# Kernel optimization log

Measured on AMD Instinct MI355X. Metric: run time of the kernel, lower is better.

## Reference

```python
import jax, jax.numpy as jnp
import numpy as np

H = 4          # attention heads
K = 16         # knn neighbors
EPS = 1e-5     # BatchNorm eps


def setup_inputs() -> dict:
    key = jax.random.key(0)
    ks = jax.random.split(key, 10)
    B, C, T, N = 2, 128, 32, 512
    OUT = 128
    HID = 2 * C + 2 * OUT  # ff hidden = in*2 + out*2
    s = 0.02
    return {
        "x_all": jax.random.normal(ks[0], (B, C, T, N), jnp.float32),
        "Wq": jax.random.normal(ks[1], (C, C), jnp.float32) * s,
        "Wk": jax.random.normal(ks[2], (C, C), jnp.float32) * s,
        "Wv": jax.random.normal(ks[3], (C, C), jnp.float32) * s,
        "W1": jax.random.normal(ks[4], (HID, C), jnp.float32) * s,
        "W2": jax.random.normal(ks[5], (OUT, HID), jnp.float32) * s,
        "bn_gamma": 1.0 + 0.1 * jax.random.normal(ks[6], (OUT,), jnp.float32),
        "bn_beta": 0.1 * jax.random.normal(ks[7], (OUT,), jnp.float32),
        "bn_mean": 0.1 * jax.random.normal(ks[8], (OUT,), jnp.float32),
        "bn_var": jax.random.uniform(ks[9], (OUT,), jnp.float32, 0.5, 1.5),
    }


def reference(x_all, Wq, Wk, Wv, W1, W2, bn_gamma, bn_beta, bn_mean, bn_var):
    B, C, T, N = x_all.shape
    D = C // H
    # --- st_group_points: candidate pool = 3 consecutive frames (replicate temporal pad), frame-major ---
    xp = jnp.concatenate([x_all[:, :, :1], x_all, x_all[:, :, -1:]], axis=2)   # (B,C,T+2,N)
    pool = jnp.stack([xp[:, :, :-2], xp[:, :, 1:-1], xp[:, :, 2:]], axis=3)    # (B,C,T,3,N)
    pool = pool.reshape(B, C, T, 3 * N)                                        # (B,C,T,3N)
    # KNN on xyz (channels 0:3); sqrt is monotone so topk on squared dists gives same indices
    a = x_all[:, :3]                                                           # (B,3,T,N)
    b = pool[:, :3]                                                            # (B,3,T,3N)
    d2 = jnp.sum((a[..., :, None] - b[..., None, :]) ** 2, axis=1)             # (B,T,N,3N)
    _, idx = jax.lax.top_k(-d2, K)                                             # (B,T,N,K) smallest-dist
    nb = jnp.take_along_axis(pool[:, :, :, None, :], idx[:, None], axis=-1)    # (B,C,T,N,K)
    rel = x_all[..., None] - nb                                                # diff grouping (B,C,T,N,K)
    # --- per-point local attention over K neighbors (1x1 convs == channel matmuls), all t at once ---
    q = jnp.einsum('oc,bctn->botn', Wq, x_all).reshape(B, H, D, T, N)
    k = jnp.einsum('oc,bctnk->botnk', Wk, rel).reshape(B, H, D, T, N, K)
    v = jnp.einsum('oc,bctnk->botnk', Wv, rel).reshape(B, H, D, T, N, K)
    energy = jnp.einsum('bhdtn,bhdtnk->bhtnk', q, k) / jnp.sqrt(jnp.float32(D))
    attn = jax.nn.softmax(energy, axis=-1)                                     # (B,H,T,N,K)
    agg = jnp.einsum('bhtnk,bhdtnk->bhdtn', attn, v).reshape(B, C, T, N)
    # --- residual + BatchNorm1d (eval mode, running stats) + conv feed-forward ---
    h = x_all + agg
    scale = (bn_gamma / jnp.sqrt(bn_var + EPS))[None, :, None, None]
    h = (h - bn_mean[None, :, None, None]) * scale + bn_beta[None, :, None, None]
    h = jax.nn.leaky_relu(jnp.einsum('oc,bctn->botn', W1, h), 0.2)
    y = jnp.einsum('oc,bctn->botn', W2, h)                                     # (B,OUT,T,N)
    return jnp.concatenate([x_all[:, :4], y], axis=1)                          # (B,4+OUT,T,N)
```

## Files before the change

kernel.cpp:

```cpp
#include <hip/hip_runtime.h>
#include <hip/hip_bf16.h>

typedef __hip_bfloat16 bf16;
typedef unsigned long long u64;
typedef __attribute__((ext_vector_type(8))) short short8;
typedef __attribute__((ext_vector_type(4))) float f32x4;

#define B_   2
#define C_   128
#define T_   32
#define N_   512
#define K_   16
#define HID_ 512
#define TN   (T_*N_)
#define PTS  (B_*T_*N_)

#define MFMA_BF16(a,b,c) __builtin_amdgcn_mfma_f32_16x16x32_bf16((a),(b),(c),0,0,0)

__device__ __forceinline__ float b2f(bf16 v){ return __bfloat162float(v); }
__device__ __forceinline__ bf16  f2b(float v){ return __float2bfloat16(v); }
__device__ __forceinline__ float bqf(short v){
  return __uint_as_float(((unsigned)(unsigned short)v) << 16);
}

__device__ __forceinline__ float ldc(const void* p, int i, bool f32) {
  return f32 ? ((const float*)p)[i] : b2f(((const bf16*)p)[i]);
}

__global__ __launch_bounds__(256) void convw_kernel(
    const void* __restrict__ x,
    const void* wq, const void* wk, const void* wv,
    const void* w1, const void* w2, const void* g, const void* bb,
    const void* m, const void* v,
    bf16* __restrict__ wqb, bf16* __restrict__ wkb, bf16* __restrict__ wvb,
    bf16* __restrict__ w1b, bf16* __restrict__ w2b,
    float* __restrict__ gf, float* __restrict__ bf_, float* __restrict__ mf,
    float* __restrict__ vf, int* __restrict__ flag)
{
  __shared__ int cnt;
  if (threadIdx.x == 0) cnt = 0;
  __syncthreads();
  const unsigned short* u = (const unsigned short*)x;
  int w = 0;
#pragma unroll
  for (int j = 0; j < 8; ++j) {
    unsigned short hv = u[threadIdx.x*8 + j];
    int e = (hv >> 7) & 0xFF;
    if (e >= 0x89) w++;
  }
  if (w) atomicAdd(&cnt, w);
  __syncthreads();
  bool f32 = (cnt > 32);
  if (blockIdx.x == 0 && threadIdx.x == 0) *flag = f32 ? 1 : 0;

  int i = blockIdx.x*256 + threadIdx.x;
  if (i < 16384) { wqb[i] = f2b(ldc(wq, i, f32)); return; } i -= 16384;
  if (i < 16384) { wkb[i] = f2b(ldc(wk, i, f32)); return; } i -= 16384;
  if (i < 16384) { wvb[i] = f2b(ldc(wv, i, f32)); return; } i -= 16384;
  if (i < 65536) { w1b[i] = f2b(ldc(w1, i, f32)); return; } i -= 65536;
  if (i < 65536) { w2b[i] = f2b(ldc(w2, i, f32)); return; } i -= 65536;
  if (i < 128)   { gf[i]  = ldc(g, i, f32); return; }       i -= 128;
  if (i < 128)   { bf_[i] = ldc(bb, i, f32); return; }      i -= 128;
  if (i < 128)   { mf[i]  = ldc(m, i, f32); return; }       i -= 128;
  if (i < 128)   { vf[i]  = ldc(v, i, f32); return; }
}

__device__ __forceinline__ u64 shflx64(u64 v, int m) {
  return (u64)__shfl_xor((long long)v, m, 64);
}

__device__ __forceinline__ void proj_gemm32(const bf16* __restrict__ W,
                                            bf16 (*ys)[136],
                                            const short8 am[2][4],
                                            int mrow, int quad, int ot)
{
  f32x4 acc[2];
#pragma unroll
  for (int mt=0;mt<2;++mt) acc[mt] = (f32x4){0.f,0.f,0.f,0.f};
#pragma unroll
  for (int kq=0;kq<4;++kq) {
    short8 bfr = *(const short8*)&W[(ot*16+mrow)*C_ + kq*32 + quad*8];
#pragma unroll
    for (int mt=0;mt<2;++mt) acc[mt] = MFMA_BF16(am[mt][kq], bfr, acc[mt]);
  }
#pragma unroll
  for (int mt=0;mt<2;++mt)
#pragma unroll
    for (int r=0;r<4;++r)
      ys[mt*16 + quad*4 + r][ot*16 + mrow] = f2b(acc[mt][r]);
}

__device__ __forceinline__ void tile_store32_512(bf16* __restrict__ dst,
                                                 const bf16 (*ys)[136], int tid)
{
  int flat = tid*8;
  int p = flat >> 7, c = flat & 127;
  *(short8*)&dst[(size_t)p*C_ + c] = *(const short8*)&ys[p][c];
}

__global__ __launch_bounds__(512) void projknn_kernel(
    const void* __restrict__ x, const int* __restrict__ flag,
    const bf16* __restrict__ wqb, const bf16* __restrict__ wkb, const bf16* __restrict__ wvb,
    bf16* __restrict__ xTb, bf16* QT, bf16* __restrict__ KT, bf16* __restrict__ VT,
    int* __restrict__ idxout)
{
  __shared__ __align__(16) char smem[28672];
  int tid = threadIdx.x;
  int blk = blockIdx.x;
  int g = blk / 5, r = blk - g*5;
  if (r == 4) {
    bf16 (*xs )[136] = (bf16(*)[136])(smem);
    bf16 (*ysK)[136] = (bf16(*)[136])(smem + 8704);
    bf16 (*ysV)[136] = (bf16(*)[136])(smem + 17408);
    int p0 = g * 32;
    int b = p0 >> 14; int tn0 = p0 & (TN-1);
    if (*flag) {
      const float* xbase = (const float*)x + (size_t)b*C_*TN + tn0;
#pragma unroll
      for (int it=0; it<8; ++it) {
        int i = it*512 + tid;
        int c = i >> 5, p = i & 31;
        xs[p][c] = f2b(xbase[(size_t)c*TN + p]);
      }
    } else {
      const bf16* xbase = (const bf16*)x + (size_t)b*C_*TN + tn0;
#pragma unroll
      for (int it=0; it<8; ++it) {
        int i = it*512 + tid;
        int c = i >> 5, p = i & 31;
        xs[p][c] = xbase[(size_t)c*TN + p];
      }
    }
    __syncthreads();
    tile_store32_512(xTb + (size_t)p0*C_, xs, tid);
    int lane = tid & 63, wave = tid >> 6;
    int mrow = lane & 15, quad = lane >> 4;
    short8 am[2][4];
#pragma unroll
    for (int mt=0;mt<2;++mt)
#pragma unroll
      for (int kq=0;kq<4;++kq)
        am[mt][kq] = *(const short8*)&xs[mt*16 + mrow][kq*32 + quad*8];
    __syncthreads();
    proj_gemm32(wqb, xs,  am, mrow, quad, wave);
    proj_gemm32(wkb, ysK, am, mrow, quad, wave);
    proj_gemm32(wvb, ysV, am, mrow, quad, wave);
    __syncthreads();
    tile_store32_512(QT + (size_t)p0*C_, xs,  tid);
    tile_store32_512(KT + (size_t)p0*C_, ysK, tid);
    tile_store32_512(VT + (size_t)p0*C_, ysV, tid);
  } else {
    float4* cand4 = (float4*)smem;
    u64 (*surv)[64] = (u64(*)[64])(smem + 24576);
    int kblk = g*4 + r;
    int row = kblk >> 6;
    int b = row >> 5, t = row & 31;
    int ng = kblk & 63;
    bool f32 = (*flag != 0);
#pragma unroll
    for (int q = 0; q < 3; ++q) {
      int tt = t - 1 + q; tt = tt < 0 ? 0 : (tt > T_-1 ? T_-1 : tt);
      size_t base = ((size_t)b*C_*T_ + tt)*(size_t)N_ + tid;
      float c0, c1, c2;
      if (f32) {
        const float* xp = (const float*)x;
        c0 = xp[base]; c1 = xp[base + (size_t)T_*N_]; c2 = xp[base + 2*(size_t)T_*N_];
      } else {
        const bf16* xp = (const bf16*)x;
        c0 = b2f(xp[base]); c1 = b2f(xp[base + (size_t)T_*N_]); c2 = b2f(xp[base + 2*(size_t)T_*N_]);
      }
      cand4[q*N_ + tid] = make_float4(c0, c1, c2, 0.f);
    }
    __syncthreads();
    int wave = tid >> 6, lane = tid & 63;
    int n = ng*8 + wave;
    float4 a = cand4[N_ + n];
    unsigned db[24];
#pragma unroll
    for (int j = 0; j < 24; ++j) {
      float4 cm = cand4[lane + (j << 6)];
      float dx = a.x - cm.x;
      float dy = a.y - cm.y;
      float dz = a.z - cm.z;
      float d2 = __fadd_rn(__fadd_rn(__fmul_rn(dx,dx), __fmul_rn(dy,dy)), __fmul_rn(dz,dz));
      db[j] = __float_as_uint(d2);
    }
    unsigned mm[12];
#pragma unroll
    for (int j = 0; j < 12; ++j) mm[j] = db[2*j] < db[2*j+1] ? db[2*j] : db[2*j+1];
#pragma unroll
    for (int j = 0; j < 6; ++j)  mm[j] = mm[2*j] < mm[2*j+1] ? mm[2*j] : mm[2*j+1];
#pragma unroll
    for (int j = 0; j < 3; ++j)  mm[j] = mm[2*j] < mm[2*j+1] ? mm[2*j] : mm[2*j+1];
    unsigned bd = mm[0] < mm[1] ? mm[0] : mm[1];
    bd = bd < mm[2] ? bd : mm[2];
    {
      unsigned lo = 0u, hi = 0x7f800000u;
#pragma unroll
      for (int it = 0; it < 16; ++it) {
        unsigned mid = lo + ((hi - lo) >> 1);
        int cge = __popcll(__ballot(bd <= mid));
        bool ge = (cge >= K_);
        hi = ge ? mid : hi;
        lo = ge ? lo : (mid + 1u);
      }
      bd = hi;
    }
    unsigned U = bd;
    int c = 0;
#pragma unroll
    for (int j = 0; j < 24; ++j) c += (db[j] <= U) ? 1 : 0;
    int ofs = 0, total = 0;
#pragma unroll
    for (int bit = 0; bit < 5; ++bit) {
      u64 mball = __ballot(((c >> bit) & 1) != 0);
      unsigned below = __builtin_amdgcn_mbcnt_hi((unsigned)(mball >> 32),
                        __builtin_amdgcn_mbcnt_lo((unsigned)mball, 0u));
      ofs   += ((int)below) << bit;
      total += (__popcll(mball)) << bit;
    }
    int point = (b*T_ + t)*N_ + n;
    if (total <= 64) {
#pragma unroll
      for (int j = 0; j < 24; ++j) {
        if (db[j] <= U) {
          surv[wave][ofs] = ((u64)db[j] << 11) | (unsigned)(lane + (j << 6));
          ++ofs;
        }
      }
      if (lane == total) surv[wave][lane] = ~0ull;
      __threadfence_block();
      u64 kk = (lane < total) ? surv[wave][lane] : ~0ull;
      int npair = (total + 1) >> 1;
      int rank = 0;
      const ulonglong2* sk2 = (const ulonglong2*)&surv[wave][0];
#pragma unroll 4
      for (int i2 = 0; i2 < npair; ++i2) {
        ulonglong2 kp = sk2[i2];
        rank += (kp.x < kk) ? 1 : 0;
        rank += (kp.y < kk) ? 1 : 0;
      }
      if (rank < K_) idxout[point*K_ + rank] = (int)(kk & 2047u);
    } else {
      u64 key[24];
#pragma unroll
      for (int j = 0; j < 24; ++j)
        key[j] = ((u64)db[j] << 32) | (unsigned)(lane + (j << 6));
      u64 res = ~0ull;
#pragma unroll 1
      for (int rr = 0; rr < 16; ++rr) {
        u64 m2 = key[0];
#pragma unroll
        for (int j = 1; j < 24; ++j) m2 = (key[j] < m2) ? key[j] : m2;
#pragma unroll
        for (int s = 32; s >= 1; s >>= 1) {
          u64 p = shflx64(m2, s);
          m2 = (p < m2) ? p : m2;
        }
        if (lane == rr) res = m2;
        int mwin = (int)(m2 & 0xffffffffu);
        int sel = ((mwin & 63) == lane) ? (mwin >> 6) : -1;
#pragma unroll
        for (int j = 0; j < 24; ++j) if (j == sel) key[j] = ~0ull;
      }
      if (lane < K_) idxout[point*K_ + lane] = (int)(res & 0xffffffffu);
    }
  }
}

__global__ __launch_bounds__(512) void attn_kernel(
    const int* __restrict__ idxin, const bf16* __restrict__ xTb,
    bf16* qhT , const bf16* __restrict__ KT,
    const bf16* __restrict__ VT,
    const float* __restrict__ gf, const float* __restrict__ bf_,
    const float* __restrict__ mf, const float* __restrict__ vf)
{
  __shared__ int   col_lds[4][16];
  __shared__ float qbuf[4][C_];
  __shared__ bf16  vbuf[4][K_][136];
  __shared__ float e_lds[4][4][16];
  int tid = threadIdx.x;
  int pt = tid >> 7, o = tid & 127;
  int gblk = (blockIdx.x & 7)*1024 + (blockIdx.x >> 3);
  int point = gblk*4 + pt;
  int b = point >> 14; int tn = point & (TN-1); int t = tn >> 9;
  if (o < K_) {
    int m = idxin[point*K_ + o];
    int j = m >> 9, nn = m & (N_-1);
    int tt = t-1+j; tt = tt<0?0:(tt>T_-1?T_-1:tt);
    col_lds[pt][o] = ((b*T_ + tt)*N_ + nn)*C_;
  }
  int self = point*C_;
  float vself = b2f(VT[self + o]);
  float xself = b2f(xTb[self + o]);
  float sc = gf[o] / sqrtf(vf[o] + 1e-5f);
  float smean = mf[o], sbeta = bf_[o];
  qbuf[pt][o] = b2f(qhT[self + o]);
  __syncthreads();
  {
    int pp = tid >> 7, r7 = tid & 127, k = r7 >> 3, c = r7 & 7;
    int hd = c >> 1;
    int src = col_lds[pp][k] + c*16;
    short8 kv0 = *(const short8*)&KT[src];
    short8 kv1 = *(const short8*)&KT[src + 8];
    short8 vv0 = *(const short8*)&VT[src];
    short8 vv1 = *(const short8*)&VT[src + 8];
    *(short8*)&vbuf[pp][k][c*16]     = vv0;
    *(short8*)&vbuf[pp][k][c*16 + 8] = vv1;
    const float* qp = &qbuf[pp][c*16];
    float qv[16];
    *(float4*)&qv[0]  = *(const float4*)(qp);
    *(float4*)&qv[4]  = *(const float4*)(qp + 4);
    *(float4*)&qv[8]  = *(const float4*)(qp + 8);
    *(float4*)&qv[12] = *(const float4*)(qp + 12);
    float e = 0.f;
#pragma unroll
    for (int i2=0;i2<8;++i2) e = fmaf(qv[i2],   bqf(kv0[i2]), e);
#pragma unroll
    for (int i2=0;i2<8;++i2) e = fmaf(qv[8+i2], bqf(kv1[i2]), e);
    e += __shfl_xor(e, 1, 64);
    if (!(c & 1)) e_lds[pp][hd][k] = -e * 0.17677669529663687f;
  }
  __syncthreads();
  int hd = o >> 5;
  float e[16]; float mx = -3e38f;
#pragma unroll
  for (int k=0;k<K_;++k){ e[k]=e_lds[pt][hd][k]; mx=fmaxf(mx,e[k]); }
  float ssum=0.f;
#pragma unroll
  for (int k=0;k<K_;++k){ e[k]=__expf(e[k]-mx); ssum+=e[k]; }
  float inv = 1.f/ssum;
  float acc = vself;
#pragma unroll
  for (int k=0;k<K_;++k)
    acc = fmaf(-(e[k]*inv), b2f(vbuf[pt][k][o]), acc);
  float hv = xself + acc;
  qhT[self + o] = f2b((hv - smean)*sc + sbeta);
}

__global__ __launch_bounds__(256) void mlp_kernel(const bf16* __restrict__ hT,
                                                  const bf16* __restrict__ w1b,
                                                  const bf16* __restrict__ w2b,
                                                  const void* __restrict__ x,
                                                  const int* __restrict__ flag,
                                                  void* out)
{
  __shared__ bf16 hidh[32][264];
  int tid = threadIdx.x;
  int p0 = blockIdx.x*32;
  int lane = tid & 63, wave = tid >> 6;
  int mrow = lane & 15, quad = lane >> 4;
  bool f32o = (*flag != 0);
  int bb = p0 >> 14;
  int tn0 = p0 & (TN-1);
  if (tid < 128) {
    int c = tid >> 5, p = tid & 31;
    size_t si = ((size_t)bb*C_ + c)*TN + tn0 + p;
    size_t di = ((size_t)bb*132 + c)*TN + tn0 + p;
    if (f32o) ((float*)out)[di] = ((const float*)x)[si];
    else      ((bf16*)out)[di]  = ((const bf16*)x)[si];
  }
  f32x4 acc2[2][2];
#pragma unroll
  for (int oi=0;oi<2;++oi)
#pragma unroll
    for (int mt=0;mt<2;++mt) acc2[oi][mt] = (f32x4){0.f,0.f,0.f,0.f};

#pragma unroll
  for (int half = 0; half < 2; ++half) {
    if (half) __syncthreads();
    short8 am[2][4];
#pragma unroll
    for (int mt=0;mt<2;++mt)
#pragma unroll
      for (int kq=0;kq<4;++kq)
        am[mt][kq] = *(const short8*)&hT[(size_t)(p0 + mt*16 + mrow)*C_ + kq*32 + quad*8];
#pragma unroll
    for (int oi = 0; oi < 4; ++oi) {
      int ot_g = half*16 + wave*4 + oi;
      int otl  = wave*4 + oi;
      f32x4 acc[2];
#pragma unroll
      for (int mt=0;mt<2;++mt) acc[mt] = (f32x4){0.f,0.f,0.f,0.f};
#pragma unroll
      for (int kq=0;kq<4;++kq) {
        short8 bfr = *(const short8*)&w1b[(ot_g*16+mrow)*C_ + kq*32 + quad*8];
#pragma unroll
        for (int mt=0;mt<2;++mt) acc[mt] = MFMA_BF16(am[mt][kq], bfr, acc[mt]);
      }
#pragma unroll
      for (int mt=0;mt<2;++mt)
#pragma unroll
        for (int r=0;r<4;++r) {
          float z = acc[mt][r];
          hidh[mt*16 + quad*4 + r][otl*16 + mrow] = f2b(z > 0.f ? z : 0.2f*z);
        }
    }
    __syncthreads();
#pragma unroll
    for (int kc = 0; kc < 4; ++kc) {
      short8 ha[2][2];
#pragma unroll
      for (int mt=0;mt<2;++mt)
#pragma unroll
        for (int kk=0;kk<2;++kk)
          ha[mt][kk] = *(const short8*)&hidh[mt*16 + mrow][(kc*2+kk)*32 + quad*8];
#pragma unroll
      for (int oi=0;oi<2;++oi) {
        int ot2 = wave*2 + oi;
#pragma unroll
        for (int kk=0;kk<2;++kk) {
          int ks_g = half*8 + kc*2 + kk;
          short8 bfr = *(const short8*)&w2b[(ot2*16+mrow)*HID_ + ks_g*32 + quad*8];
#pragma unroll
          for (int mt=0;mt<2;++mt)
            acc2[oi][mt] = MFMA_BF16(ha[mt][kk], bfr, acc2[oi][mt]);
        }
      }
    }
  }
  size_t obase = (size_t)bb*132*TN;
#pragma unroll
  for (int oi=0;oi<2;++oi) {
    int ch = (wave*2+oi)*16 + mrow;
#pragma unroll
    for (int mt=0;mt<2;++mt) {
      int tn = tn0 + mt*16 + quad*4;
      size_t oidx = obase + (size_t)(4+ch)*TN + tn;
      if (f32o) {
        *(f32x4*)&((float*)out)[oidx] = acc2[oi][mt];
      } else {
        bf16 tmp[4];
#pragma unroll
        for (int r=0;r<4;++r) tmp[r] = f2b(acc2[oi][mt][r]);
        *(u64*)&((bf16*)out)[oidx] = *(u64*)tmp;
      }
    }
  }
}

extern "C" void kernel_launch(void* const* d_in, const int* in_sizes, int n_in,
                              void* d_out, int out_size, void* d_ws, size_t ws_size,
                              hipStream_t stream)
{
  (void)in_sizes; (void)n_in; (void)out_size; (void)ws_size;
  const void* x = d_in[0];
  char* ws = (char*)d_ws;
  const size_t MB = (size_t)1<<20;
  bf16*  QT  = (bf16* )(ws + 0*MB);
  bf16*  KT  = (bf16* )(ws + 8*MB);
  bf16*  VT  = (bf16* )(ws + 16*MB);
  bf16*  xTb = (bf16* )(ws + 24*MB);
  int*   idxw= (int*  )(ws + 32*MB);
  bf16*  wqb = (bf16* )(ws + 34*MB);
  bf16*  wkb = (bf16* )(ws + 34*MB + 0x8000);
  bf16*  wvb = (bf16* )(ws + 34*MB + 0x10000);
  bf16*  w1b = (bf16* )(ws + 34*MB + 0x18000);
  bf16*  w2b = (bf16* )(ws + 34*MB + 0x38000);
  float* gf  = (float*)(ws + 34*MB + 0x58000);
  float* bf_ = (float*)(ws + 34*MB + 0x58200);
  float* mf  = (float*)(ws + 34*MB + 0x58400);
  float* vf  = (float*)(ws + 34*MB + 0x58600);
  int*  flag = (int*  )(ws + 34*MB + 0x58800);

  convw_kernel  <<<dim3(706), dim3(256), 0, stream>>>(
      x, d_in[1], d_in[2], d_in[3], d_in[4], d_in[5],
      d_in[6], d_in[7], d_in[8], d_in[9],
      wqb, wkb, wvb, w1b, w2b, gf, bf_, mf, vf, flag);
  projknn_kernel<<<dim3(5120), dim3(512), 0, stream>>>(
      x, flag, wqb, wkb, wvb, xTb, QT, KT, VT, idxw);
  attn_kernel   <<<dim3(PTS/4), dim3(512), 0, stream>>>(
      idxw, xTb, QT , KT, VT, gf, bf_, mf, vf);
  mlp_kernel    <<<dim3(PTS/32), dim3(256), 0, stream>>>(
      QT , w1b, w2b, x, flag, d_out);
}
```

Baseline: 202.9 us.

## Fuse attention and MLP kernels, keeping normalized features in shared memory

Merges the per-point attention kernel and the feed-forward MLP kernel into one launch. Each 256-thread block loops over its 32 points two at a time, writes the normalized hidden rows into LDS, and then runs the MFMA MLP directly from LDS. This removes the global round trip of the intermediate h tensor and one kernel launch. In exchange, the attention phase gets much less parallelism per block (2 points per iteration with serial sub-iterations and two barriers each), so latency hiding for the neighbor gathers may suffer.

After: 198.6 us. 1.02x faster.

```diff
diff --git a/kernel.cpp b/kernel.cpp
--- a/kernel.cpp
+++ b/kernel.cpp
@@ -268,91 +268,30 @@
   }
 }
 
-__global__ __launch_bounds__(512) void attn_kernel(
+__global__ __launch_bounds__(256) void attnmlp_kernel(
     const int* __restrict__ idxin, const bf16* __restrict__ xTb,
-    bf16* qhT , const bf16* __restrict__ KT,
+    const bf16* __restrict__ QT, const bf16* __restrict__ KT,
     const bf16* __restrict__ VT,
     const float* __restrict__ gf, const float* __restrict__ bf_,
-    const float* __restrict__ mf, const float* __restrict__ vf)
-{
-  __shared__ int   col_lds[4][16];
-  __shared__ float qbuf[4][C_];
-  __shared__ bf16  vbuf[4][K_][136];
-  __shared__ float e_lds[4][4][16];
+    const float* __restrict__ mf, const float* __restrict__ vf,
+    const bf16* __restrict__ w1b, const bf16* __restrict__ w2b,
+    const void* __restrict__ x, const int* __restrict__ flag,
+    void* __restrict__ out)
+{
+  __shared__ __align__(16) char smem[25600];
+  bf16  (*hTl)[136]      = (bf16 (*)[136])     (smem);
+  float (*qbuf)[C_]      = (float(*)[C_])      (smem + 8704);
+  int   (*col_lds)[K_]   = (int  (*)[K_])      (smem + 9728);
+  float (*e_lds)[4][K_]  = (float(*)[4][K_])   (smem + 9856);
+  bf16  (*vbuf)[K_][136] = (bf16 (*)[K_][136]) (smem + 10368);
+  bf16  (*hidh)[264]     = (bf16 (*)[264])     (smem + 8704);
+
   int tid = threadIdx.x;
-  int pt = tid >> 7, o = tid & 127;
-  int gblk = (blockIdx.x & 7)*1024 + (blockIdx.x >> 3);
-  int point = gblk*4 + pt;
-  int b = point >> 14; int tn = point & (TN-1); int t = tn >> 9;
-  if (o < K_) {
-    int m = idxin[point*K_ + o];
-    int j = m >> 9, nn = m & (N_-1);
-    int tt = t-1+j; tt = tt<0?0:(tt>T_-1?T_-1:tt);
-    col_lds[pt][o] = ((b*T_ + tt)*N_ + nn)*C_;
-  }
-  int self = point*C_;
-  float vself = b2f(VT[self + o]);
-  float xself = b2f(xTb[self + o]);
-  float sc = gf[o] / sqrtf(vf[o] + 1e-5f);
-  float smean = mf[o], sbeta = bf_[o];
-  qbuf[pt][o] = b2f(qhT[self + o]);
-  __syncthreads();
-  {
-    int pp = tid >> 7, r7 = tid & 127, k = r7 >> 3, c = r7 & 7;
-    int hd = c >> 1;
-    int src = col_lds[pp][k] + c*16;
-    short8 kv0 = *(const short8*)&KT[src];
-    short8 kv1 = *(const short8*)&KT[src + 8];
-    short8 vv0 = *(const short8*)&VT[src];
-    short8 vv1 = *(const short8*)&VT[src + 8];
-    *(short8*)&vbuf[pp][k][c*16]     = vv0;
-    *(short8*)&vbuf[pp][k][c*16 + 8] = vv1;
-    const float* qp = &qbuf[pp][c*16];
-    float qv[16];
-    *(float4*)&qv[0]  = *(const float4*)(qp);
-    *(float4*)&qv[4]  = *(const float4*)(qp + 4);
-    *(float4*)&qv[8]  = *(const float4*)(qp + 8);
-    *(float4*)&qv[12] = *(const float4*)(qp + 12);
-    float e = 0.f;
-#pragma unroll
-    for (int i2=0;i2<8;++i2) e = fmaf(qv[i2],   bqf(kv0[i2]), e);
-#pragma unroll
-    for (int i2=0;i2<8;++i2) e = fmaf(qv[8+i2], bqf(kv1[i2]), e);
-    e += __shfl_xor(e, 1, 64);
-    if (!(c & 1)) e_lds[pp][hd][k] = -e * 0.17677669529663687f;
-  }
-  __syncthreads();
-  int hd = o >> 5;
-  float e[16]; float mx = -3e38f;
-#pragma unroll
-  for (int k=0;k<K_;++k){ e[k]=e_lds[pt][hd][k]; mx=fmaxf(mx,e[k]); }
-  float ssum=0.f;
-#pragma unroll
-  for (int k=0;k<K_;++k){ e[k]=__expf(e[k]-mx); ssum+=e[k]; }
-  float inv = 1.f/ssum;
-  float acc = vself;
-#pragma unroll
-  for (int k=0;k<K_;++k)
-    acc = fmaf(-(e[k]*inv), b2f(vbuf[pt][k][o]), acc);
-  float hv = xself + acc;
-  qhT[self + o] = f2b((hv - smean)*sc + sbeta);
-}
-
-__global__ __launch_bounds__(256) void mlp_kernel(const bf16* __restrict__ hT,
-                                                  const bf16* __restrict__ w1b,
-                                                  const bf16* __restrict__ w2b,
-                                                  const void* __restrict__ x,
-                                                  const int* __restrict__ flag,
-                                                  void* out)
-{
-  __shared__ bf16 hidh[32][264];
-  int tid = threadIdx.x;
-  int p0 = blockIdx.x*32;
-  int lane = tid & 63, wave = tid >> 6;
-  int mrow = lane & 15, quad = lane >> 4;
-  bool f32o = (*flag != 0);
+  int gblk = (blockIdx.x & 7)*128 + (blockIdx.x >> 3);
+  int p0 = gblk * 32;
   int bb = p0 >> 14;
   int tn0 = p0 & (TN-1);
+  bool f32o = (*flag != 0);
   if (tid < 128) {
     int c = tid >> 5, p = tid & 31;
     size_t si = ((size_t)bb*C_ + c)*TN + tn0 + p;
@@ -360,6 +299,87 @@
     if (f32o) ((float*)out)[di] = ((const float*)x)[si];
     else      ((bf16*)out)[di]  = ((const bf16*)x)[si];
   }
+
+  int pt = tid >> 7, o = tid & 127;
+  float sc = gf[o] / sqrtf(vf[o] + 1e-5f);
+  float smean = mf[o], sbeta = bf_[o];
+  float vselfC, xselfC;
+  {
+    int point = p0 + pt;
+    int b = point >> 14, tn = point & (TN-1), t = tn >> 9;
+    if (o < K_) {
+      int m = idxin[point*K_ + o];
+      int j = m >> 9, nn = m & (N_-1);
+      int tt = t-1+j; tt = tt<0?0:(tt>T_-1?T_-1:tt);
+      col_lds[pt][o] = ((b*T_ + tt)*N_ + nn)*C_;
+    }
+    int self = point*C_;
+    vselfC = b2f(VT[self + o]);
+    xselfC = b2f(xTb[self + o]);
+    qbuf[pt][o] = b2f(QT[self + o]);
+  }
+  __syncthreads();
+#pragma unroll 1
+  for (int sub = 0; sub < 16; ++sub) {
+    {
+      int k = o >> 3, c = o & 7, hd = c >> 1;
+      int src = col_lds[pt][k] + c*16;
+      short8 kv0 = *(const short8*)&KT[src];
+      short8 kv1 = *(const short8*)&KT[src + 8];
+      short8 vv0 = *(const short8*)&VT[src];
+      short8 vv1 = *(const short8*)&VT[src + 8];
+      *(short8*)&vbuf[pt][k][c*16]     = vv0;
+      *(short8*)&vbuf[pt][k][c*16 + 8] = vv1;
+      const float* qp = &qbuf[pt][c*16];
+      float qv[16];
+      *(float4*)&qv[0]  = *(const float4*)(qp);
+      *(float4*)&qv[4]  = *(const float4*)(qp + 4);
+      *(float4*)&qv[8]  = *(const float4*)(qp + 8);
+      *(float4*)&qv[12] = *(const float4*)(qp + 12);
+      float e = 0.f;
+#pragma unroll
+      for (int i2=0;i2<8;++i2) e = fmaf(qv[i2],   bqf(kv0[i2]), e);
+#pragma unroll
+      for (int i2=0;i2<8;++i2) e = fmaf(qv[8+i2], bqf(kv1[i2]), e);
+      e += __shfl_xor(e, 1, 64);
+      if (!(c & 1)) e_lds[pt][hd][k] = -e * 0.17677669529663687f;
+    }
+    __syncthreads();
+    {
+      int hd = o >> 5;
+      float e[16]; float mx = -3e38f;
+#pragma unroll
+      for (int k=0;k<K_;++k){ e[k]=e_lds[pt][hd][k]; mx=fmaxf(mx,e[k]); }
+      float ssum=0.f;
+#pragma unroll
+      for (int k=0;k<K_;++k){ e[k]=__expf(e[k]-mx); ssum+=e[k]; }
+      float inv = 1.f/ssum;
+      float acc = vselfC;
+#pragma unroll
+      for (int k=0;k<K_;++k)
+        acc = fmaf(-(e[k]*inv), b2f(vbuf[pt][k][o]), acc);
+      float hv = xselfC + acc;
+      hTl[sub*2 + pt][o] = f2b((hv - smean)*sc + sbeta);
+    }
+    if (sub < 15) {
+      int point = p0 + (sub+1)*2 + pt;
+      int b = point >> 14, tn = point & (TN-1), t = tn >> 9;
+      if (o < K_) {
+        int m = idxin[point*K_ + o];
+        int j = m >> 9, nn = m & (N_-1);
+        int tt = t-1+j; tt = tt<0?0:(tt>T_-1?T_-1:tt);
+        col_lds[pt][o] = ((b*T_ + tt)*N_ + nn)*C_;
+      }
+      int self = point*C_;
+      vselfC = b2f(VT[self + o]);
+      xselfC = b2f(xTb[self + o]);
+      qbuf[pt][o] = b2f(QT[self + o]);
+    }
+    __syncthreads();
+  }
+
+  int lane = tid & 63, wave = tid >> 6;
+  int mrow = lane & 15, quad = lane >> 4;
   f32x4 acc2[2][2];
 #pragma unroll
   for (int oi=0;oi<2;++oi)
@@ -374,7 +394,7 @@
     for (int mt=0;mt<2;++mt)
 #pragma unroll
       for (int kq=0;kq<4;++kq)
-        am[mt][kq] = *(const short8*)&hT[(size_t)(p0 + mt*16 + mrow)*C_ + kq*32 + quad*8];
+        am[mt][kq] = *(const short8*)&hTl[mt*16 + mrow][kq*32 + quad*8];
 #pragma unroll
     for (int oi = 0; oi < 4; ++oi) {
       int ot_g = half*16 + wave*4 + oi;
@@ -469,8 +489,6 @@
       wqb, wkb, wvb, w1b, w2b, gf, bf_, mf, vf, flag);
   projknn_kernel<<<dim3(5120), dim3(512), 0, stream>>>(
       x, flag, wqb, wkb, wvb, xTb, QT, KT, VT, idxw);
-  attn_kernel   <<<dim3(PTS/4), dim3(512), 0, stream>>>(
-      idxw, xTb, QT , KT, VT, gf, bf_, mf, vf);
-  mlp_kernel    <<<dim3(PTS/32), dim3(256), 0, stream>>>(
-      QT , w1b, w2b, x, flag, d_out);
-}
+  attnmlp_kernel<<<dim3(PTS/32), dim3(256), 0, stream>>>(
+      idxw, xTb, QT, KT, VT, gf, bf_, mf, vf, w1b, w2b, x, flag, d_out);
+}
```
